# Kernel tuning notes

Hardware: AMD Instinct MI355X
Metric: run time of the kernel (lower is better)

The kernel has to match this reference:

```python
import jax, jax.numpy as jnp
import numpy as np

D_MODEL = 1024


def setup_inputs() -> dict:
    key = jax.random.key(0)
    k1, k2, k3 = jax.random.split(key, 3)
    x = jax.random.normal(k1, (4, 2048, D_MODEL), dtype=jnp.float32)
    w_qkv = jax.random.normal(k2, (D_MODEL, 3 * D_MODEL), dtype=jnp.float32) * (D_MODEL ** -0.5)
    b_qkv = jnp.zeros((3 * D_MODEL,), dtype=jnp.float32)
    w_out = jax.random.normal(k3, (D_MODEL, D_MODEL), dtype=jnp.float32) * (D_MODEL ** -0.5)
    b_out = jnp.zeros((D_MODEL,), dtype=jnp.float32)
    return {"x": x, "w_qkv": w_qkv, "b_qkv": b_qkv, "w_out": w_out, "b_out": b_out}


def reference(x, w_qkv, b_qkv, w_out, b_out):
    # x: [B, S, D]
    d_model = x.shape[-1]
    scale = jnp.asarray(d_model, x.dtype) ** 0.5
    qkv = x @ w_qkv + b_qkv                      # [B, S, 3D]
    q, k, v = jnp.split(qkv, 3, axis=-1)          # each [B, S, D]
    scores = jnp.einsum('bsd,btd->bst', q, k) / scale  # [B, S, S]
    attn = jax.nn.softmax(scores, axis=-1)
    out = jnp.einsum('bst,btd->bsd', attn, v)     # [B, S, D]
    return out @ w_out + b_out
```

## Files before the change

### kernel.cpp

```cpp
#include <hip/hip_runtime.h>
#include <hip/hip_bf16.h>
#include <cstdint>

typedef __attribute__((ext_vector_type(8))) short bf16x8;
typedef __attribute__((ext_vector_type(4))) float f32x4;
using bf16 = __hip_bfloat16;

static __device__ __forceinline__ void storeval(float* p, float v) { *p = v; }
static __device__ __forceinline__ void storeval(bf16* p, float v) { *p = __float2bfloat16(v); }

#define MFMA_BF16 __builtin_amdgcn_mfma_f32_16x16x32_bf16

template <int N>
static __device__ __forceinline__ void vm_wait() {
    if constexpr (N == 0) asm volatile("s_waitcnt vmcnt(0)" ::: "memory");
    else if constexpr (N == 6) asm volatile("s_waitcnt vmcnt(6)" ::: "memory");
    else if constexpr (N == 8) asm volatile("s_waitcnt vmcnt(8)" ::: "memory");
}
static __device__ __forceinline__ void bar() { __builtin_amdgcn_s_barrier(); }
static __device__ __forceinline__ void sb() { __builtin_amdgcn_sched_barrier(0xF); }
static __device__ __forceinline__ void gl_lds(const bf16* src, char* dst) {
    __builtin_amdgcn_global_load_lds((const __attribute__((address_space(1))) unsigned int*)src,
                                     (__attribute__((address_space(3))) unsigned int*)dst, 16, 0, 0);
}

__global__ __launch_bounds__(256) void prep(const float* __restrict__ x, bf16* __restrict__ xb,
                                            const float* __restrict__ w_qkv, bf16* __restrict__ wqkvT,
                                            const float* __restrict__ w_out, bf16* __restrict__ woutT) {
    __shared__ float tile[32][33];
    const int b = blockIdx.x;
    const int tid = threadIdx.x;
    if (b < 4096) {
        long i = ((long)b * 256 + tid) * 8;
        float4 a = *(const float4*)(x + i);
        float4 c = *(const float4*)(x + i + 4);
        bf16 t[8];
        t[0] = __float2bfloat16(a.x); t[1] = __float2bfloat16(a.y);
        t[2] = __float2bfloat16(a.z); t[3] = __float2bfloat16(a.w);
        t[4] = __float2bfloat16(c.x); t[5] = __float2bfloat16(c.y);
        t[6] = __float2bfloat16(c.z); t[7] = __float2bfloat16(c.w);
        *(uint4*)(xb + i) = *(const uint4*)t;
        return;
    }
    const float* src; bf16* dst; long ss, ds; int tx, ty;
    if (b < 7168) {
        int ib = b - 4096;
        tx = ib % 96; ty = ib / 96;
        src = w_qkv; dst = wqkvT; ss = 3072; ds = 1024;
    } else {
        int ib = b - 7168;
        tx = ib & 31; ty = ib >> 5;
        src = w_out; dst = woutT; ss = 1024; ds = 1024;
    }
    long r0 = (long)ty * 32, c0 = (long)tx * 32;
    int lx = tid & 31, ly = tid >> 5;
    for (int i = ly; i < 32; i += 8)
        tile[i][lx] = src[(r0 + i) * ss + c0 + lx];
    __syncthreads();
    for (int i = ly; i < 32; i += 8)
        dst[(c0 + i) * ds + r0 + lx] = __float2bfloat16(tile[lx][i]);
}

template <typename OutT, bool BIAS, int BM>
__global__ __launch_bounds__(512, 1) void gemm_sp(
    const bf16* __restrict__ Ag, long lda, long batchA,
    const bf16* __restrict__ Bg, long ldb, long batchB,
    OutT* __restrict__ Cg, long ldc, long batchC,
    const float* __restrict__ bias, int K, float alpha, int nx, int ny) {
    constexpr int MR = BM / 32;
    constexpr int A_HP = (BM == 256) ? 16384 : 4096;
    constexpr int A_W = (BM == 256) ? 32768 : 16384;
    constexpr int A_REG = BM * 256;
    constexpr int WVP = 4 + BM / 64;
    extern __shared__ __align__(16) char smem[];

    const int tid = threadIdx.x;
    const int wave = tid >> 6, lane = tid & 63, l16 = lane & 15, lhi = lane >> 4;
    const int wm = wave >> 2, wn = wave & 3;

    const int nwg = gridDim.x;
    const int l = (blockIdx.x & 7) * (nwg >> 3) + (blockIdx.x >> 3);
    const int pt = nx * ny;
    const int z = l / pt, rr = l % pt;
    const long mtile = (long)(rr / nx) * BM;
    const long ntile = (long)(rr % nx) * 256;

    const bf16* A = Ag + (long)z * batchA;
    const bf16* B = Bg + (long)z * batchB;
    OutT* C = Cg + (long)z * batchC;

    const int rp0 = tid >> 3;
    const int g8 = ((tid & 7) ^ ((tid >> 4) & 7)) * 8;
    const bf16* pA = A + (mtile + rp0) * lda + g8;
    const bf16* pB = B + (ntile + rp0) * ldb + g8;
    const int wb = wave * 1024;

    auto stageB = [&](int par, int t) {
        const bf16* s0 = pB + (long)t * 64;
        char* d0 = smem + A_REG + par * 16384 + wb;
        gl_lds(s0, d0);
        gl_lds(s0 + 64 * ldb, d0 + 8192);
        const bf16* s1 = s0 + 128 * ldb;
        char* d1 = smem + A_REG + 32768 + par * 16384 + wb;
        gl_lds(s1, d1);
        gl_lds(s1 + 64 * ldb, d1 + 8192);
    };
    auto stageA = [&](int par, int t) {
        const bf16* s0 = pA + (long)t * 64;
#pragma unroll
        for (int q = 0; q < BM / 64; ++q)
            gl_lds(s0 + q * 64 * lda, smem + q * 16384 + par * 8192 + wb);
    };

    const int swz = (l16 >> 1) & 7;
    const int cb0 = (lhi ^ swz) * 16;
    const int cb1 = ((4 + lhi) ^ swz) * 16;
    const char* aBase = smem + wm * A_W + l16 * 128;
    const char* bBase = smem + A_REG + (wn >> 1) * 32768 + ((wn & 1) * 64 + l16) * 128;

    bf16x8 aqA[MR], aqB[MR], bq[8];
    f32x4 acc[MR][4];
#pragma unroll
    for (int m = 0; m < MR; ++m)
#pragma unroll
        for (int n = 0; n < 4; ++n) acc[m][n] = f32x4{0.f, 0.f, 0.f, 0.f};

#define RD_A(AQ, par, hp)                                                      \
    do {                                                                       \
        const char* p_ = aBase + (par) * 8192 + (hp) * A_HP;                   \
        _Pragma("unroll")                                                      \
        for (int j_ = 0; j_ < MR / 2; ++j_) {                                  \
            AQ[2 * j_]     = *(const bf16x8*)(p_ + j_ * 2048 + cb0);           \
            AQ[2 * j_ + 1] = *(const bf16x8*)(p_ + j_ * 2048 + cb1);           \
        }                                                                      \
    } while (0)

#define RD_B(par, nlo)                                                         \
    do {                                                                       \
        const char* p_ = bBase + (par) * 16384 + (nlo) * 2048;                 \
        bq[(nlo) * 2 + 0] = *(const bf16x8*)(p_ + cb0);                        \
        bq[(nlo) * 2 + 1] = *(const bf16x8*)(p_ + cb1);                        \
        bq[(nlo) * 2 + 2] = *(const bf16x8*)(p_ + 2048 + cb0);                 \
        bq[(nlo) * 2 + 3] = *(const bf16x8*)(p_ + 2048 + cb1);                 \
    } while (0)

#define QUAD_(AQ, h, nlo)                                                      \
    do {                                                                       \
        __builtin_amdgcn_s_setprio(1);                                         \
        _Pragma("unroll")                                                      \
        for (int m_ = 0; m_ < MR / 2; ++m_) {                                  \
            acc[(h) * (MR / 2) + m_][(nlo) + 0] =                              \
                MFMA_BF16(AQ[2*m_], bq[(nlo)*2 + 0], acc[(h)*(MR/2) + m_][(nlo) + 0], 0, 0, 0); \
            acc[(h) * (MR / 2) + m_][(nlo) + 1] =                              \
                MFMA_BF16(AQ[2*m_], bq[(nlo)*2 + 2], acc[(h)*(MR/2) + m_][(nlo) + 1], 0, 0, 0); \
        }                                                                      \
        _Pragma("unroll")                                                      \
        for (int m_ = 0; m_ < MR / 2; ++m_) {                                  \
            acc[(h) * (MR / 2) + m_][(nlo) + 0] =                              \
                MFMA_BF16(AQ[2*m_ + 1], bq[(nlo)*2 + 1], acc[(h)*(MR/2) + m_][(nlo) + 0], 0, 0, 0); \
            acc[(h) * (MR / 2) + m_][(nlo) + 1] =                              \
                MFMA_BF16(AQ[2*m_ + 1], bq[(nlo)*2 + 3], acc[(h)*(MR/2) + m_][(nlo) + 1], 0, 0, 0); \
        }                                                                      \
        __builtin_amdgcn_s_setprio(0);                                         \
    } while (0)

#define KT(par, tstage, MODE)                                                  \
    do {                                                                       \
                                                    \
        bar(); sb();                                                           \
        QUAD_(aqA, 0, 0);                                                      \
        RD_B(par, 2);                                                          \
                                                    \
        bar(); sb();                                                           \
        QUAD_(aqA, 0, 2);                                                      \
        RD_A(aqB, par, 1);                                                     \
        vm_wait<0>();       \
                               \
        bar(); sb();             \
        QUAD_(aqB, 1, 2);                                                      \
        if (MODE < 2) RD_A(aqA, (par) ^ 1, 0);                                 \
        if (MODE == 0) stageB(par, tstage);                                    \
          \
        bar(); sb();                                                           \
        QUAD_(aqB, 1, 0);                                                      \
        if (MODE < 2) RD_B((par) ^ 1, 0);                                      \
        if (MODE == 0) stageA(par, tstage);                                    \
    } while (0)

    const int NT = K / 64;

    stageB(0, 0); stageA(0, 0);
    stageB(1, 1); stageA(1, 1);
    vm_wait<WVP>();
    bar(); sb();
    RD_A(aqA, 0, 0);
    RD_B(0, 0);

    for (int t = 0; t < NT - 2; ++t) KT(t & 1, t + 2, 0);
    KT(0, 0, 1);
    KT(1, 0, 2);

#pragma unroll
    for (int n = 0; n < 4; ++n) {
        long col = ntile + wn * 64 + n * 16 + l16;
        float bv = BIAS ? bias[col] : 0.0f;
#pragma unroll
        for (int am = 0; am < MR; ++am) {
            const int h_ = am / (MR / 2), mm = am % (MR / 2);
            long row = mtile + wm * (BM / 2) + h_ * (BM / 4) + mm * 16 + lhi * 4;
#pragma unroll
            for (int r2 = 0; r2 < 4; ++r2)
                storeval(&C[(row + r2) * ldc + col], acc[am][n][r2] * alpha + bv);
        }
    }
#undef KT
#undef QUAD_
#undef RD_B
#undef RD_A
}

__global__ __launch_bounds__(256) void softmax_vtrans(bf16* __restrict__ sc,
                                                      const bf16* __restrict__ qkv,
                                                      bf16* __restrict__ vt) {
    const int b = blockIdx.x;
    const int tid = threadIdx.x;
    if (b < 8192) {
        __shared__ float red[8];
        bf16* srow = sc + (long)b * 2048;
        uint4 raw = *(const uint4*)(srow + tid * 8);
        const bf16* rb = (const bf16*)&raw;
        float v[8];
#pragma unroll
        for (int j = 0; j < 8; ++j) v[j] = __bfloat162float(rb[j]);
        float m = -3.4e38f;
#pragma unroll
        for (int j = 0; j < 8; ++j) m = fmaxf(m, v[j]);
#pragma unroll
        for (int off = 32; off; off >>= 1) m = fmaxf(m, __shfl_xor(m, off));
        if ((tid & 63) == 0) red[tid >> 6] = m;
        __syncthreads();
        m = fmaxf(fmaxf(red[0], red[1]), fmaxf(red[2], red[3]));
        float s = 0.0f;
#pragma unroll
        for (int j = 0; j < 8; ++j) {
            v[j] = __expf(v[j] - m);
            s += v[j];
        }
#pragma unroll
        for (int off = 32; off; off >>= 1) s += __shfl_xor(s, off);
        if ((tid & 63) == 0) red[4 + (tid >> 6)] = s;
        __syncthreads();
        s = red[4] + red[5] + red[6] + red[7];
        float inv = 1.0f / s;
        bf16 o[8];
#pragma unroll
        for (int j = 0; j < 8; ++j) o[j] = __float2bfloat16(v[j] * inv);
        *(uint4*)(srow + tid * 8) = *(const uint4*)o;
        return;
    }
    __shared__ float tile[32][33];
    const int ib = b - 8192;
    const int z = ib >> 11;
    const int rem = ib & 2047;
    const int tx = rem & 31;
    const int ty = rem >> 5;
    const bf16* s = qkv + 2048 + (long)z * 2048 * 3072;
    bf16* d = vt + (long)z * 1024 * 2048;
    long r0 = (long)ty * 32, c0 = (long)tx * 32;
    int lx = tid & 31, ly = tid >> 5;
    for (int i = ly; i < 32; i += 8)
        tile[i][lx] = __bfloat162float(s[(r0 + i) * 3072 + c0 + lx]);
    __syncthreads();
    for (int i = ly; i < 32; i += 8)
        d[(c0 + i) * 2048 + r0 + lx] = __float2bfloat16(tile[lx][i]);
}

extern "C" void kernel_launch(void* const* d_in, const int* in_sizes, int n_in, void* d_out,
                              int out_size, void* d_ws, size_t ws_size, hipStream_t stream) {
    (void)in_sizes; (void)n_in; (void)out_size; (void)ws_size;
    const float* x = (const float*)d_in[0];
    const float* w_qkv = (const float*)d_in[1];
    const float* b_qkv = (const float*)d_in[2];
    const float* w_out = (const float*)d_in[3];
    const float* b_out = (const float*)d_in[4];
    float* out = (float*)d_out;

    const int B = 4, S = 2048, D = 1024;

    {
        (void)hipFuncSetAttribute((const void*)&gemm_sp<bf16, true, 128>,
                                  hipFuncAttributeMaxDynamicSharedMemorySize, 98304);
        (void)hipFuncSetAttribute((const void*)&gemm_sp<bf16, false, 256>,
                                  hipFuncAttributeMaxDynamicSharedMemorySize, 131072);
        (void)hipFuncSetAttribute((const void*)&gemm_sp<bf16, false, 128>,
                                  hipFuncAttributeMaxDynamicSharedMemorySize, 98304);
        (void)hipFuncSetAttribute((const void*)&gemm_sp<float, true, 128>,
                                  hipFuncAttributeMaxDynamicSharedMemorySize, 98304);
    }

    char* ws = (char*)d_ws;
    size_t off = 0;
    auto alloc = [&](size_t bytes) {
        char* p = ws + off;
        off += (bytes + 255) & ~(size_t)255;
        return p;
    };
    bf16* xb = (bf16*)alloc((size_t)B * S * D * 2);
    bf16* qkv = (bf16*)alloc((size_t)B * S * 3 * D * 2);
    bf16* wqkvT = (bf16*)alloc((size_t)3 * D * D * 2);
    bf16* woutT = (bf16*)alloc((size_t)D * D * 2);
    bf16* vt = (bf16*)alloc((size_t)B * D * S * 2);
    bf16* ao = (bf16*)alloc((size_t)B * S * D * 2);
    bf16* sc = (bf16*)alloc((size_t)B * S * S * 2);

    prep<<<8192, 256, 0, stream>>>(x, xb, w_qkv, wqkvT, w_out, woutT);

    gemm_sp<bf16, true, 128><<<768, 512, 98304, stream>>>(
        xb, D, 0, wqkvT, D, 0, qkv, 3 * D, 0, b_qkv, D, 1.0f, 3 * D / 256, B * S / 128);

    gemm_sp<bf16, false, 256><<<256, 512, 131072, stream>>>(
        qkv, 3 * D, (long)S * 3 * D, qkv + D, 3 * D, (long)S * 3 * D,
        sc, S, (long)S * S, nullptr, D, 0.03125f, S / 256, S / 256);

    softmax_vtrans<<<16384, 256, 0, stream>>>(sc, qkv, vt);

    gemm_sp<bf16, false, 128><<<256, 512, 98304, stream>>>(
        sc, S, (long)S * S, vt, S, (long)D * S,
        ao, D, (long)S * D, nullptr, S, 1.0f, D / 256, S / 128);

    gemm_sp<float, true, 128><<<256, 512, 98304, stream>>>(
        ao, D, 0, woutT, D, 0, out, D, 0, b_out, D, 1.0f, D / 256, B * S / 128);
}
```

Before: 194.7 us.

## Add triple-buffered GEMM variant for 128-row tiles with deeper prefetch

```diff
diff --git a/kernel.cpp b/kernel.cpp
--- a/kernel.cpp
+++ b/kernel.cpp
@@ -16,6 +16,7 @@
     if constexpr (N == 0) asm volatile("s_waitcnt vmcnt(0)" ::: "memory");
     else if constexpr (N == 6) asm volatile("s_waitcnt vmcnt(6)" ::: "memory");
     else if constexpr (N == 8) asm volatile("s_waitcnt vmcnt(8)" ::: "memory");
+    else if constexpr (N == 12) asm volatile("s_waitcnt vmcnt(12)" ::: "memory");
 }
 static __device__ __forceinline__ void bar() { __builtin_amdgcn_s_barrier(); }
 static __device__ __forceinline__ void sb() { __builtin_amdgcn_sched_barrier(0xF); }
@@ -61,6 +62,166 @@
         dst[(c0 + i) * ds + r0 + lx] = __float2bfloat16(tile[lx][i]);
 }
 
+template <typename OutT, bool BIAS>
+__global__ __launch_bounds__(512, 1) void gemm_tp(
+    const bf16* __restrict__ Ag, long lda, long batchA,
+    const bf16* __restrict__ Bg, long ldb, long batchB,
+    OutT* __restrict__ Cg, long ldc, long batchC,
+    const float* __restrict__ bias, int K, float alpha, int nx, int ny) {
+    extern __shared__ __align__(16) char smem[];
+
+    const int tid = threadIdx.x;
+    const int wave = tid >> 6, lane = tid & 63, l16 = lane & 15, lhi = lane >> 4;
+    const int wm = wave >> 2, wn = wave & 3;
+
+    const int nwg = gridDim.x;
+    const int l = (blockIdx.x & 7) * (nwg >> 3) + (blockIdx.x >> 3);
+    const int pt = nx * ny;
+    const int z = l / pt, rr = l % pt;
+    const long mtile = (long)(rr / nx) * 128;
+    const long ntile = (long)(rr % nx) * 256;
+
+    const bf16* A = Ag + (long)z * batchA;
+    const bf16* B = Bg + (long)z * batchB;
+    OutT* C = Cg + (long)z * batchC;
+
+    const int rp0 = tid >> 3;
+    const int g8 = ((tid & 7) ^ ((tid >> 4) & 7)) * 8;
+    const bf16* pA = A + (mtile + rp0) * lda + g8;
+    const bf16* pB = B + (ntile + rp0) * ldb + g8;
+    const int wb = wave * 1024;
+
+    auto stageB = [&](int par, int t) {
+        const bf16* s0 = pB + (long)t * 64;
+        char* d0 = smem + 49152 + par * 16384 + wb;
+        gl_lds(s0, d0);
+        gl_lds(s0 + 64 * ldb, d0 + 8192);
+        const bf16* s1 = s0 + 128 * ldb;
+        char* d1 = smem + 49152 + 49152 + par * 16384 + wb;
+        gl_lds(s1, d1);
+        gl_lds(s1 + 64 * ldb, d1 + 8192);
+    };
+    auto stageA = [&](int par, int t) {
+        const bf16* s0 = pA + (long)t * 64;
+        gl_lds(s0, smem + par * 8192 + wb);
+        gl_lds(s0 + 64 * lda, smem + 24576 + par * 8192 + wb);
+    };
+
+    const int swz = (l16 >> 1) & 7;
+    const int cb0 = (lhi ^ swz) * 16;
+    const int cb1 = ((4 + lhi) ^ swz) * 16;
+    const char* aBase = smem + wm * 24576 + l16 * 128;
+    const char* bBase = smem + 49152 + (wn >> 1) * 49152 + ((wn & 1) * 64 + l16) * 128;
+
+    bf16x8 aqA[4], aqB[4], bq[8];
+    f32x4 acc[4][4];
+#pragma unroll
+    for (int m = 0; m < 4; ++m)
+#pragma unroll
+        for (int n = 0; n < 4; ++n) acc[m][n] = f32x4{0.f, 0.f, 0.f, 0.f};
+
+#define RD_A(AQ, par, hp)                                                      \
+    do {                                                                       \
+        const char* p_ = aBase + (par) * 8192 + (hp) * 4096;                   \
+        AQ[0] = *(const bf16x8*)(p_ + cb0);                                    \
+        AQ[1] = *(const bf16x8*)(p_ + cb1);                                    \
+        AQ[2] = *(const bf16x8*)(p_ + 2048 + cb0);                             \
+        AQ[3] = *(const bf16x8*)(p_ + 2048 + cb1);                             \
+    } while (0)
+
+#define RD_B(par, nlo)                                                         \
+    do {                                                                       \
+        const char* p_ = bBase + (par) * 16384 + (nlo) * 2048;                 \
+        bq[(nlo) * 2 + 0] = *(const bf16x8*)(p_ + cb0);                        \
+        bq[(nlo) * 2 + 1] = *(const bf16x8*)(p_ + cb1);                        \
+        bq[(nlo) * 2 + 2] = *(const bf16x8*)(p_ + 2048 + cb0);                 \
+        bq[(nlo) * 2 + 3] = *(const bf16x8*)(p_ + 2048 + cb1);                 \
+    } while (0)
+
+#define QUAD_(AQ, h, nlo)                                                      \
+    do {                                                                       \
+        __builtin_amdgcn_s_setprio(1);                                         \
+        _Pragma("unroll")                                                      \
+        for (int m_ = 0; m_ < 2; ++m_) {                                       \
+            acc[(h)*2 + m_][(nlo) + 0] =                                       \
+                MFMA_BF16(AQ[2*m_], bq[(nlo)*2 + 0], acc[(h)*2 + m_][(nlo) + 0], 0, 0, 0); \
+            acc[(h)*2 + m_][(nlo) + 1] =                                       \
+                MFMA_BF16(AQ[2*m_], bq[(nlo)*2 + 2], acc[(h)*2 + m_][(nlo) + 1], 0, 0, 0); \
+        }                                                                      \
+        _Pragma("unroll")                                                      \
+        for (int m_ = 0; m_ < 2; ++m_) {                                       \
+            acc[(h)*2 + m_][(nlo) + 0] =                                       \
+                MFMA_BF16(AQ[2*m_ + 1], bq[(nlo)*2 + 1], acc[(h)*2 + m_][(nlo) + 0], 0, 0, 0); \
+            acc[(h)*2 + m_][(nlo) + 1] =                                       \
+                MFMA_BF16(AQ[2*m_ + 1], bq[(nlo)*2 + 3], acc[(h)*2 + m_][(nlo) + 1], 0, 0, 0); \
+        }                                                                      \
+        __builtin_amdgcn_s_setprio(0);                                         \
+    } while (0)
+
+#define KT(par, parN, tstage, MODE)                                            \
+    do {                                                                       \
+                                                    \
+        bar(); sb();                                                           \
+        QUAD_(aqA, 0, 0);                                                      \
+        RD_B(par, 2);                                                          \
+                                                    \
+        bar(); sb();                                                           \
+        QUAD_(aqA, 0, 2);                                                      \
+        RD_A(aqB, par, 1);                                                     \
+        if (MODE == 0 || MODE == 3) vm_wait<6>();                              \
+        if (MODE == 1) vm_wait<0>();                                           \
+                               \
+        bar(); sb();                                                           \
+        QUAD_(aqB, 1, 2);                                                      \
+        if (MODE != 2) RD_A(aqA, parN, 0);                                     \
+        if (MODE == 0) stageB(par, tstage);                                    \
+                          \
+        bar(); sb();                                                           \
+        QUAD_(aqB, 1, 0);                                                      \
+        if (MODE != 2) RD_B(parN, 0);                                          \
+        if (MODE == 0) stageA(par, tstage);                                    \
+    } while (0)
+
+    const int NT = K / 64;
+
+    stageB(0, 0); stageA(0, 0);
+    stageB(1, 1); stageA(1, 1);
+    stageB(2, 2); stageA(2, 2);
+    vm_wait<12>();
+    bar(); sb();
+    RD_A(aqA, 0, 0);
+    RD_B(0, 0);
+
+    int par = 0, parN = 1;
+    for (int t = 0; t < NT - 3; ++t) {
+        KT(par, parN, t + 3, 0);
+        par = parN; parN = (parN == 2) ? 0 : parN + 1;
+    }
+    KT(par, parN, 0, 3);
+    par = parN; parN = (parN == 2) ? 0 : parN + 1;
+    KT(par, parN, 0, 1);
+    par = parN;
+    KT(par, 0, 0, 2);
+
+#pragma unroll
+    for (int n = 0; n < 4; ++n) {
+        long col = ntile + wn * 64 + n * 16 + l16;
+        float bv = BIAS ? bias[col] : 0.0f;
+#pragma unroll
+        for (int am = 0; am < 4; ++am) {
+            const int h_ = am >> 1, mm = am & 1;
+            long row = mtile + wm * 64 + h_ * 32 + mm * 16 + lhi * 4;
+#pragma unroll
+            for (int r2 = 0; r2 < 4; ++r2)
+                storeval(&C[(row + r2) * ldc + col], acc[am][n][r2] * alpha + bv);
+        }
+    }
+#undef KT
+#undef QUAD_
+#undef RD_B
+#undef RD_A
+}
+
 template <typename OutT, bool BIAS, int BM>
 __global__ __launch_bounds__(512, 1) void gemm_sp(
     const bf16* __restrict__ Ag, long lda, long batchA,
@@ -166,21 +327,17 @@
 
 #define KT(par, tstage, MODE)                                                  \
     do {                                                                       \
-                                                    \
         bar(); sb();                                                           \
         QUAD_(aqA, 0, 0);                                                      \
         RD_B(par, 2);                                                          \
-                                                    \
         bar(); sb();                                                           \
         QUAD_(aqA, 0, 2);                                                      \
         RD_A(aqB, par, 1);                                                     \
-        vm_wait<0>();       \
-                               \
-        bar(); sb();             \
+        vm_wait<0>();                                                          \
+        bar(); sb();                                                           \
         QUAD_(aqB, 1, 2);                                                      \
         if (MODE < 2) RD_A(aqA, (par) ^ 1, 0);                                 \
         if (MODE == 0) stageB(par, tstage);                                    \
-          \
         bar(); sb();                                                           \
         QUAD_(aqB, 1, 0);                                                      \
         if (MODE < 2) RD_B((par) ^ 1, 0);                                      \
@@ -288,14 +445,14 @@
     const int B = 4, S = 2048, D = 1024;
 
     {
-        (void)hipFuncSetAttribute((const void*)&gemm_sp<bf16, true, 128>,
-                                  hipFuncAttributeMaxDynamicSharedMemorySize, 98304);
+        (void)hipFuncSetAttribute((const void*)&gemm_tp<bf16, true>,
+                                  hipFuncAttributeMaxDynamicSharedMemorySize, 147456);
+        (void)hipFuncSetAttribute((const void*)&gemm_tp<bf16, false>,
+                                  hipFuncAttributeMaxDynamicSharedMemorySize, 147456);
+        (void)hipFuncSetAttribute((const void*)&gemm_tp<float, true>,
+                                  hipFuncAttributeMaxDynamicSharedMemorySize, 147456);
         (void)hipFuncSetAttribute((const void*)&gemm_sp<bf16, false, 256>,
                                   hipFuncAttributeMaxDynamicSharedMemorySize, 131072);
-        (void)hipFuncSetAttribute((const void*)&gemm_sp<bf16, false, 128>,
-                                  hipFuncAttributeMaxDynamicSharedMemorySize, 98304);
-        (void)hipFuncSetAttribute((const void*)&gemm_sp<float, true, 128>,
-                                  hipFuncAttributeMaxDynamicSharedMemorySize, 98304);
     }
 
     char* ws = (char*)d_ws;
@@ -315,7 +472,7 @@
 
     prep<<<8192, 256, 0, stream>>>(x, xb, w_qkv, wqkvT, w_out, woutT);
 
-    gemm_sp<bf16, true, 128><<<768, 512, 98304, stream>>>(
+    gemm_tp<bf16, true><<<768, 512, 147456, stream>>>(
         xb, D, 0, wqkvT, D, 0, qkv, 3 * D, 0, b_qkv, D, 1.0f, 3 * D / 256, B * S / 128);
 
     gemm_sp<bf16, false, 256><<<256, 512, 131072, stream>>>(
@@ -324,10 +481,10 @@
 
     softmax_vtrans<<<16384, 256, 0, stream>>>(sc, qkv, vt);
 
-    gemm_sp<bf16, false, 128><<<256, 512, 98304, stream>>>(
+    gemm_tp<bf16, false><<<256, 512, 147456, stream>>>(
         sc, S, (long)S * S, vt, S, (long)D * S,
         ao, D, (long)S * D, nullptr, S, 1.0f, D / 256, S / 128);
 
-    gemm_sp<float, true, 128><<<256, 512, 98304, stream>>>(
+    gemm_tp<float, true><<<256, 512, 147456, stream>>>(
         ao, D, 0, woutT, D, 0, out, D, 0, b_out, D, 1.0f, D / 256, B * S / 128);
 }
```

After: 196.6 us. Within noise of the previous version (+1.0%).
